# Kernel tuning notes

Hardware: AMD Instinct MI355X
Metric: run time of the kernel (lower is better)

Reference implementation:

```python
import jax, jax.numpy as jnp
import numpy as np

B, T, C = 8, 2048, 1024  # batch, seq_len (== block_size), n_embed
HEAD = 64


def setup_inputs() -> dict:
    key = jax.random.key(0)
    k1, k2, k3, k4 = jax.random.split(key, 4)
    x = jax.random.normal(k1, (B, T, C), dtype=jnp.float32)
    # nn.Linear(n_embed, head_size, bias=False) -> weight [head, C]; stored as [C, head]
    Wk = jax.random.normal(k2, (C, HEAD), dtype=jnp.float32) * (C ** -0.5)
    Wq = jax.random.normal(k3, (C, HEAD), dtype=jnp.float32) * (C ** -0.5)
    Wv = jax.random.normal(k4, (C, HEAD), dtype=jnp.float32) * (C ** -0.5)
    return {"x": x, "Wk": Wk, "Wq": Wq, "Wv": Wv}


def reference(x, Wk, Wq, Wv):
    Bx, Tx, Cx = x.shape
    k = jnp.einsum('btc,ch->bth', x, Wk)  # [B,T,HEAD]
    q = jnp.einsum('btc,ch->bth', x, Wq)
    v = jnp.einsum('btc,ch->bth', x, Wv)
    # Source quirk: scores = k @ q^T (k rows), scaled by n_embed**-0.5 (C, not head_size)
    scores = jnp.einsum('bih,bjh->bij', k, q) * (Cx ** -0.5)  # [B,T,T]
    causal = jnp.tril(jnp.ones((Tx, Tx), dtype=bool))
    scores = jnp.where(causal, scores, -jnp.inf)
    attn = jax.nn.softmax(scores, axis=-1)
    out = jnp.einsum('bij,bjh->bih', attn, v)  # [B,T,HEAD]
    return out
```

## Files before the change

### kernel.cpp

```cpp
#include <hip/hip_runtime.h>
#include <cstdint>

#define B_ 8
#define T_ 2048
#define C_ 1024
#define H_ 64
#define BT_ (B_ * T_)

typedef short short8 __attribute__((ext_vector_type(8)));
typedef short bh4 __attribute__((ext_vector_type(4)));
typedef float f32x4 __attribute__((ext_vector_type(4)));

__device__ inline short f2bf(float f) {
  uint32_t u = __float_as_uint(f);
  u += 0x7fffu + ((u >> 16) & 1u);
  return (short)(u >> 16);
}

__device__ __forceinline__ void gl_lds16(const void* g, void* l) {
  __builtin_amdgcn_global_load_lds(
      (const __attribute__((address_space(1))) unsigned int*)g,
      (__attribute__((address_space(3))) unsigned int*)l, 16, 0, 0);
}

#define ALOADO(dst, p, off)                                        \
  asm volatile("global_load_dwordx4 %0, %1, off offset:" #off      \
               : "=v"(dst) : "v"(p) : "memory")

__global__ __launch_bounds__(256) void prep_w(
    const float* __restrict__ Wk, const float* __restrict__ Wq,
    const float* __restrict__ Wv, short* __restrict__ Wp) {
  __shared__ float wl[64][68];
  const int mat = blockIdx.x >> 4;
  const int kc = blockIdx.x & 15;
  const float* W = (mat == 0) ? Wk : (mat == 1) ? Wq : Wv;
  const float sc = (mat == 0) ? 0.03125f * 1.44269504088896f : 1.0f;
  const int t = threadIdx.x;
  const int k0 = kc * 64;
#pragma unroll
  for (int j = 0; j < 4; ++j) {
    int s = t + 256 * j;
    int kr = s >> 4, cf = s & 15;
    float4 v = *reinterpret_cast<const float4*>(&W[(size_t)(k0 + kr) * H_ + cf * 4]);
    wl[kr][cf * 4 + 0] = v.x; wl[kr][cf * 4 + 1] = v.y;
    wl[kr][cf * 4 + 2] = v.z; wl[kr][cf * 4 + 3] = v.w;
  }
  __syncthreads();
#pragma unroll
  for (int j = 0; j < 2; ++j) {
    int s = t + 256 * j;
    int n = s >> 3, g = s & 7;
    short8 o;
#pragma unroll
    for (int i = 0; i < 8; ++i) o[i] = f2bf(wl[8 * g + i][n] * sc);
    const int ng = mat * 64 + n;
    const int nt = ng >> 4, l15c = ng & 15;
    const int f = g >> 2, lg2 = g & 3;
    short* dst = Wp + (((size_t)(kc * 12 + nt) * 2 + f) << 9) +
                 ((lg2 << 4) + l15c) * 8;
    *reinterpret_cast<short8*>(dst) = o;
  }
}

__global__ __launch_bounds__(256, 1) void proj_kernel(
    const float* __restrict__ x, const short* __restrict__ Wp,
    short* __restrict__ Kp, short* __restrict__ Qp, short* __restrict__ Vt) {
  __shared__ float xs[2][32 * 64];
  const int t = threadIdx.x;
  const int w = t >> 6, lane = t & 63;
  const int l15 = lane & 15, lg = lane >> 4;
  const int rg = w >> 1, ch = w & 1;
  const int rowBase = blockIdx.x * 32;

  f32x4 acc[6];
  const f32x4 zf = {0.f, 0.f, 0.f, 0.f};
#pragma unroll
  for (int i = 0; i < 6; ++i) acc[i] = zf;

  auto stageX = [&](int buf, int k0) {
#pragma unroll
    for (int j = 0; j < 2; ++j) {
      const int seg = w * 2 + j;
      const int r = seg * 4 + (lane >> 4);
      const float* g =
          &x[(size_t)(rowBase + r) * C_ + k0 + (((lane & 15) ^ (r & 7)) << 2)];
      gl_lds16(g, (char*)&xs[buf][0] + seg * 1024);
    }
  };

  stageX(0, 0);

#pragma unroll 1
  for (int it = 0; it < 16; ++it) {
    __syncthreads();
    const int cb = it & 1;
    short8 bw[12];
    const short* wb0 = Wp + (((size_t)(it * 12 + 6 * ch)) << 10) + lane * 8;
    const short* wb1 = wb0 + 2048;
    const short* wb2 = wb0 + 4096;
    ALOADO(bw[0], wb0, 0);    ALOADO(bw[1], wb0, 1024);
    ALOADO(bw[2], wb0, 2048); ALOADO(bw[3], wb0, 3072);
    ALOADO(bw[4], wb1, 0);    ALOADO(bw[5], wb1, 1024);
    ALOADO(bw[6], wb1, 2048); ALOADO(bw[7], wb1, 3072);
    ALOADO(bw[8], wb2, 0);    ALOADO(bw[9], wb2, 1024);
    ALOADO(bw[10], wb2, 2048); ALOADO(bw[11], wb2, 3072);
    __builtin_amdgcn_sched_barrier(0);
    if (it < 15) stageX(cb ^ 1, (it + 1) * 64);
    __builtin_amdgcn_sched_barrier(0);
    if (it < 15) {
      asm volatile("s_waitcnt vmcnt(2)" ::: "memory");
    } else {
      asm volatile("s_waitcnt vmcnt(0)" ::: "memory");
    }
    __builtin_amdgcn_sched_barrier(0);

    const int arow = 16 * rg + l15;
    const int x7 = arow & 7;
    const float* xrow = &xs[cb][arow * 64];
    float4 fa = *reinterpret_cast<const float4*>(xrow + (((2 * lg) ^ x7) << 2));
    float4 fb = *reinterpret_cast<const float4*>(xrow + (((2 * lg + 1) ^ x7) << 2));
    float4 fc = *reinterpret_cast<const float4*>(xrow + (((2 * lg + 8) ^ x7) << 2));
    float4 fd = *reinterpret_cast<const float4*>(xrow + (((2 * lg + 9) ^ x7) << 2));
    short8 a0, a1;
    a0[0] = f2bf(fa.x); a0[1] = f2bf(fa.y); a0[2] = f2bf(fa.z); a0[3] = f2bf(fa.w);
    a0[4] = f2bf(fb.x); a0[5] = f2bf(fb.y); a0[6] = f2bf(fb.z); a0[7] = f2bf(fb.w);
    a1[0] = f2bf(fc.x); a1[1] = f2bf(fc.y); a1[2] = f2bf(fc.z); a1[3] = f2bf(fc.w);
    a1[4] = f2bf(fd.x); a1[5] = f2bf(fd.y); a1[6] = f2bf(fd.z); a1[7] = f2bf(fd.w);
#pragma unroll
    for (int nt = 0; nt < 6; ++nt) {
      acc[nt] = __builtin_amdgcn_mfma_f32_16x16x32_bf16(a0, bw[2 * nt], acc[nt], 0, 0, 0);
      acc[nt] = __builtin_amdgcn_mfma_f32_16x16x32_bf16(a1, bw[2 * nt + 1], acc[nt], 0, 0, 0);
    }
  }

  const int strip = blockIdx.x * 2 + rg;
  const int rb = strip * 16;
#pragma unroll
  for (int nt = 0; nt < 6; ++nt) {
    const int ntg = 6 * ch + nt;
    if (ntg < 8) {
      short* O = (ntg < 4) ? Kp : Qp;
      const int col = (ntg & 3) * 16 + l15;
#pragma unroll
      for (int r = 0; r < 4; ++r)
        O[(size_t)(rb + lg * 4 + r) * H_ + col] = f2bf(acc[nt][r]);
    }
  }
  __syncthreads();
  if (ch == 1) {
    short* vl = reinterpret_cast<short*>(&xs[0][0]) + rg * (16 * 66);
#pragma unroll
    for (int nt = 2; nt < 6; ++nt)
#pragma unroll
      for (int r = 0; r < 4; ++r)
        vl[(lg * 4 + r) * 66 + (nt - 2) * 16 + l15] = f2bf(acc[nt][r]);
    asm volatile("s_waitcnt lgkmcnt(0)" ::: "memory");
    short8 o0, o1;
#pragma unroll
    for (int i = 0; i < 8; ++i) o0[i] = vl[i * 66 + lane];
#pragma unroll
    for (int i = 0; i < 8; ++i) o1[i] = vl[(8 + i) * 66 + lane];
    const int bb = strip >> 7, tb = (strip & 127) * 16;
    short* dst = &Vt[((size_t)bb * H_ + lane) * T_ + tb];
    *reinterpret_cast<short8*>(dst) = o0;
    *reinterpret_cast<short8*>(dst + 8) = o1;
  }
}

__global__ __launch_bounds__(512) void attn_kernel(
    const short* __restrict__ Kq, const short* __restrict__ Qk,
    const short* __restrict__ Vt, float* __restrict__ Pg,
    float* __restrict__ Mg) {
  __shared__ short Ks[4][64 * 64];
  __shared__ short Vs[4][64 * 64];
  const int t = threadIdx.x, w = t >> 6, lane = t & 63;
  const int l15 = lane & 15, lg = lane >> 4;
  const int batch = blockIdx.x & 7;
  const int rest = blockIdx.x >> 3;
  const int qh = rest & 3;
  const int g = rest >> 2;
  const int sidx = (g < 8) ? (15 - g) : (g - 8);
  const int rg = w;
  const short* Kb = Kq + (size_t)batch * T_ * H_;
  const short* Qb = Qk + (size_t)batch * T_ * H_;
  const short* Vb = Vt + (size_t)batch * H_ * T_;
  const f32x4 zf = {0.f, 0.f, 0.f, 0.f};
  const int k7 = l15 & 7;

  const int qbase = sidx * 128;
  const int qrow = qbase + rg * 16 + l15;
  const short8 qa0 = *reinterpret_cast<const short8*>(&Kb[(size_t)qrow * H_ + lg * 8]);
  const short8 qa1 = *reinterpret_cast<const short8*>(&Kb[(size_t)qrow * H_ + lg * 8 + 32]);
  const int ntop = 2 * sidx + 1;
  const int nlist = (ntop >= qh) ? (((ntop - qh) >> 2) + 1) : 0;
  const int np = (nlist + 1) >> 1;

  const int tp = w >> 2, kind = (w >> 1) & 1, q2 = w & 1;
  const int srow = lane >> 3;
  const int ssw = ((lane & 7) ^ srow) << 3;
  auto stage = [&](int per) {
    const int le = 2 * per + tp;
    if (le >= nlist) return;
    const int gkt = 4 * le + qh;
    const int buf = (per & 1) * 2 + tp;
    const int kbase = gkt * 64;
    if (kind == 0) {
#pragma unroll
      for (int g2 = 0; g2 < 4; ++g2) {
        const int gg = q2 * 4 + g2;
        gl_lds16(&Qb[(size_t)(kbase + gg * 8 + srow) * H_ + ssw],
                 (char*)&Ks[buf][0] + gg * 1024);
      }
    } else {
#pragma unroll
      for (int g2 = 0; g2 < 4; ++g2) {
        const int gg = q2 * 4 + g2;
        gl_lds16(&Vb[(size_t)(gg * 8 + srow) * T_ + kbase + ssw],
                 (char*)&Vs[buf][0] + gg * 1024);
      }
    }
  };

  f32x4 O[4];
#pragma unroll
  for (int i = 0; i < 4; ++i) O[i] = zf;
  float m = -1e30f, l = 0.f;

  stage(0);

#pragma unroll 1
  for (int i = 0; i < np; ++i) {
    __syncthreads();
    if (i + 1 < np) stage(i + 1);
#pragma unroll 1
    for (int tt = 0; tt < 2; ++tt) {
      const int le = 2 * i + tt;
      if (le < nlist) {
        const int gkt = 4 * le + qh;
        const int cb = (i & 1) * 2 + tt;
        const int kbase = gkt * 64;
        f32x4 S[4];
        __builtin_amdgcn_s_setprio(1);
#pragma unroll
        for (int nt = 0; nt < 4; ++nt) {
          S[nt] = zf;
          const short* krow = &Ks[cb][(16 * nt + l15) * 64];
          short8 kf0 = *reinterpret_cast<const short8*>(&krow[(lg ^ k7) << 3]);
          short8 kf1 = *reinterpret_cast<const short8*>(&krow[((4 + lg) ^ k7) << 3]);
          S[nt] = __builtin_amdgcn_mfma_f32_16x16x32_bf16(kf0, qa0, S[nt], 0, 0, 0);
          S[nt] = __builtin_amdgcn_mfma_f32_16x16x32_bf16(kf1, qa1, S[nt], 0, 0, 0);
        }
        __builtin_amdgcn_s_setprio(0);
        if (gkt >= 2 * sidx) {
#pragma unroll
          for (int nt = 0; nt < 4; ++nt) {
            const int klo = kbase + 16 * nt + 4 * lg;
#pragma unroll
            for (int r = 0; r < 4; ++r)
              if (klo + r > qrow) S[nt][r] = -1e30f;
          }
        }
        float mx0 = fmaxf(fmaxf(S[0][0], S[0][1]), fmaxf(S[0][2], S[0][3]));
        float mx1 = fmaxf(fmaxf(S[1][0], S[1][1]), fmaxf(S[1][2], S[1][3]));
        float mx2 = fmaxf(fmaxf(S[2][0], S[2][1]), fmaxf(S[2][2], S[2][3]));
        float mx3 = fmaxf(fmaxf(S[3][0], S[3][1]), fmaxf(S[3][2], S[3][3]));
        float mx = fmaxf(fmaxf(mx0, mx1), fmaxf(mx2, mx3));
        mx = fmaxf(mx, __shfl_xor(mx, 16));
        mx = fmaxf(mx, __shfl_xor(mx, 32));
        const float mn = fmaxf(m, mx);
        const float scv = exp2f(m - mn);
        m = mn;
        float rs = 0.f;
#pragma unroll
        for (int nt = 0; nt < 4; ++nt)
#pragma unroll
          for (int r = 0; r < 4; ++r) {
            const float pv = exp2f(S[nt][r] - mn);
            S[nt][r] = pv;
            rs += pv;
          }
        rs += __shfl_xor(rs, 16);
        rs += __shfl_xor(rs, 32);
        l = l * scv + rs;
#pragma unroll
        for (int nt = 0; nt < 4; ++nt) O[nt] *= scv;
        const int d7 = l15 & 7;
        const int vo = 4 * (lg & 1);
        __builtin_amdgcn_s_setprio(1);
#pragma unroll
        for (int kc = 0; kc < 2; ++kc) {
          short8 pa;
#pragma unroll
          for (int jj = 0; jj < 8; ++jj)
            pa[jj] = f2bf(S[2 * kc + (jj >> 2)][jj & 3]);
          const int slo = ((4 * kc + (lg >> 1)) ^ d7) << 3;
          const int shi = ((4 * kc + 2 + (lg >> 1)) ^ d7) << 3;
#pragma unroll
          for (int nt = 0; nt < 4; ++nt) {
            const short* vrow = &Vs[cb][(16 * nt + l15) * 64];
            const bh4 vlo = *reinterpret_cast<const bh4*>(&vrow[slo + vo]);
            const bh4 vhi = *reinterpret_cast<const bh4*>(&vrow[shi + vo]);
            short8 vf;
            vf[0] = vlo[0]; vf[1] = vlo[1]; vf[2] = vlo[2]; vf[3] = vlo[3];
            vf[4] = vhi[0]; vf[5] = vhi[1]; vf[6] = vhi[2]; vf[7] = vhi[3];
            O[nt] = __builtin_amdgcn_mfma_f32_16x16x32_bf16(vf, pa, O[nt], 0, 0, 0);
          }
        }
        __builtin_amdgcn_s_setprio(0);
      }
    }
  }

  const size_t gr = (size_t)batch * T_ + qrow;
#pragma unroll
  for (int nt = 0; nt < 4; ++nt)
    *reinterpret_cast<f32x4*>(&Pg[((size_t)qh * BT_ + gr) * H_ + 16 * nt + 4 * lg]) = O[nt];
  if (lg == 0) {
    Mg[((size_t)qh * BT_ + gr) * 2 + 0] = m;
    Mg[((size_t)qh * BT_ + gr) * 2 + 1] = l;
  }
}

__global__ __launch_bounds__(256) void combine_kernel(
    const float* __restrict__ Pg, const float* __restrict__ Mg,
    float* __restrict__ out) {
  const int t = threadIdx.x;
#pragma unroll
  for (int k = 0; k < 2; ++k) {
    const int task = blockIdx.x * 512 + k * 256 + t;
    const int row = task >> 4;
    const int c4 = task & 15;
    float Mh[4], Lh[4];
#pragma unroll
    for (int h = 0; h < 4; ++h) {
      Mh[h] = Mg[((size_t)h * BT_ + row) * 2 + 0];
      Lh[h] = Mg[((size_t)h * BT_ + row) * 2 + 1];
    }
    const float M = fmaxf(fmaxf(Mh[0], Mh[1]), fmaxf(Mh[2], Mh[3]));
    float L = 0.f;
    f32x4 o = {0.f, 0.f, 0.f, 0.f};
#pragma unroll
    for (int h = 0; h < 4; ++h) {
      const float e = exp2f(Mh[h] - M);
      L += Lh[h] * e;
      const f32x4 po =
          *reinterpret_cast<const f32x4*>(&Pg[((size_t)h * BT_ + row) * H_ + c4 * 4]);
      o += po * e;
    }
    const f32x4 res = o * (1.f / L);
    *reinterpret_cast<f32x4*>(&out[(size_t)row * H_ + c4 * 4]) = res;
  }
}

extern "C" void kernel_launch(void* const* d_in, const int* in_sizes, int n_in,
                              void* d_out, int out_size, void* d_ws, size_t ws_size,
                              hipStream_t stream) {
  const float* x = (const float*)d_in[0];
  const float* Wk = (const float*)d_in[1];
  const float* Wq = (const float*)d_in[2];
  const float* Wv = (const float*)d_in[3];
  float* out = (float*)d_out;

  short* Kp = (short*)d_ws;
  short* Qp = Kp + (size_t)BT_ * H_;
  short* Vt = Qp + (size_t)BT_ * H_;
  short* Wp = Vt + (size_t)BT_ * H_;
  float* Pg = (float*)(Wp + 192 * C_);
  float* Mg = Pg + (size_t)4 * BT_ * H_;

  hipLaunchKernelGGL(prep_w, dim3(48), dim3(256), 0, stream, Wk, Wq, Wv, Wp);
  hipLaunchKernelGGL(proj_kernel, dim3(512), dim3(256), 0, stream, x, Wp, Kp, Qp, Vt);
  hipLaunchKernelGGL(attn_kernel, dim3(512), dim3(512), 0, stream, Kp, Qp, Vt, Pg, Mg);
  hipLaunchKernelGGL(combine_kernel, dim3(512), dim3(256), 0, stream, Pg, Mg, out);
}
```

Measured before the change: 50.33 us.

## Split projection blocks to 16 rows so each wave owns three N tiles

```diff
diff --git a/kernel.cpp b/kernel.cpp
--- a/kernel.cpp
+++ b/kernel.cpp
@@ -65,27 +65,24 @@
 __global__ __launch_bounds__(256, 1) void proj_kernel(
     const float* __restrict__ x, const short* __restrict__ Wp,
     short* __restrict__ Kp, short* __restrict__ Qp, short* __restrict__ Vt) {
-  __shared__ float xs[2][32 * 64];
+  __shared__ float xs[2][16 * 64];
   const int t = threadIdx.x;
   const int w = t >> 6, lane = t & 63;
   const int l15 = lane & 15, lg = lane >> 4;
-  const int rg = w >> 1, ch = w & 1;
-  const int rowBase = blockIdx.x * 32;
-
-  f32x4 acc[6];
+  const int ch = w;
+  const int rowBase = blockIdx.x * 16;
+
+  f32x4 acc[3];
   const f32x4 zf = {0.f, 0.f, 0.f, 0.f};
 #pragma unroll
-  for (int i = 0; i < 6; ++i) acc[i] = zf;
+  for (int i = 0; i < 3; ++i) acc[i] = zf;
 
   auto stageX = [&](int buf, int k0) {
-#pragma unroll
-    for (int j = 0; j < 2; ++j) {
-      const int seg = w * 2 + j;
-      const int r = seg * 4 + (lane >> 4);
-      const float* g =
-          &x[(size_t)(rowBase + r) * C_ + k0 + (((lane & 15) ^ (r & 7)) << 2)];
-      gl_lds16(g, (char*)&xs[buf][0] + seg * 1024);
-    }
+    const int seg = w;
+    const int r = seg * 4 + (lane >> 4);
+    const float* g =
+        &x[(size_t)(rowBase + r) * C_ + k0 + (((lane & 15) ^ (r & 7)) << 2)];
+    gl_lds16(g, (char*)&xs[buf][0] + seg * 1024);
   };
 
   stageX(0, 0);
@@ -94,27 +91,23 @@
   for (int it = 0; it < 16; ++it) {
     __syncthreads();
     const int cb = it & 1;
-    short8 bw[12];
-    const short* wb0 = Wp + (((size_t)(it * 12 + 6 * ch)) << 10) + lane * 8;
-    const short* wb1 = wb0 + 2048;
-    const short* wb2 = wb0 + 4096;
-    ALOADO(bw[0], wb0, 0);    ALOADO(bw[1], wb0, 1024);
-    ALOADO(bw[2], wb0, 2048); ALOADO(bw[3], wb0, 3072);
-    ALOADO(bw[4], wb1, 0);    ALOADO(bw[5], wb1, 1024);
-    ALOADO(bw[6], wb1, 2048); ALOADO(bw[7], wb1, 3072);
-    ALOADO(bw[8], wb2, 0);    ALOADO(bw[9], wb2, 1024);
-    ALOADO(bw[10], wb2, 2048); ALOADO(bw[11], wb2, 3072);
+    short8 bw[6];
+    const short* wb = Wp + (((size_t)(it * 12 + 3 * ch)) << 10) + lane * 8;
+    const short* wb2 = wb + 2048;
+    ALOADO(bw[0], wb, 0);    ALOADO(bw[1], wb, 1024);
+    ALOADO(bw[2], wb, 2048); ALOADO(bw[3], wb, 3072);
+    ALOADO(bw[4], wb2, 0);   ALOADO(bw[5], wb2, 1024);
     __builtin_amdgcn_sched_barrier(0);
     if (it < 15) stageX(cb ^ 1, (it + 1) * 64);
     __builtin_amdgcn_sched_barrier(0);
     if (it < 15) {
-      asm volatile("s_waitcnt vmcnt(2)" ::: "memory");
+      asm volatile("s_waitcnt vmcnt(1)" ::: "memory");
     } else {
       asm volatile("s_waitcnt vmcnt(0)" ::: "memory");
     }
     __builtin_amdgcn_sched_barrier(0);
 
-    const int arow = 16 * rg + l15;
+    const int arow = l15;
     const int x7 = arow & 7;
     const float* xrow = &xs[cb][arow * 64];
     float4 fa = *reinterpret_cast<const float4*>(xrow + (((2 * lg) ^ x7) << 2));
@@ -127,34 +120,32 @@
     a1[0] = f2bf(fc.x); a1[1] = f2bf(fc.y); a1[2] = f2bf(fc.z); a1[3] = f2bf(fc.w);
     a1[4] = f2bf(fd.x); a1[5] = f2bf(fd.y); a1[6] = f2bf(fd.z); a1[7] = f2bf(fd.w);
 #pragma unroll
-    for (int nt = 0; nt < 6; ++nt) {
+    for (int nt = 0; nt < 3; ++nt) {
       acc[nt] = __builtin_amdgcn_mfma_f32_16x16x32_bf16(a0, bw[2 * nt], acc[nt], 0, 0, 0);
       acc[nt] = __builtin_amdgcn_mfma_f32_16x16x32_bf16(a1, bw[2 * nt + 1], acc[nt], 0, 0, 0);
     }
   }
 
-  const int strip = blockIdx.x * 2 + rg;
+  const int strip = blockIdx.x;
   const int rb = strip * 16;
-#pragma unroll
-  for (int nt = 0; nt < 6; ++nt) {
-    const int ntg = 6 * ch + nt;
+  __shared__ short vl[16 * 66];
+#pragma unroll
+  for (int nt = 0; nt < 3; ++nt) {
+    const int ntg = 3 * ch + nt;
     if (ntg < 8) {
       short* O = (ntg < 4) ? Kp : Qp;
       const int col = (ntg & 3) * 16 + l15;
 #pragma unroll
       for (int r = 0; r < 4; ++r)
         O[(size_t)(rb + lg * 4 + r) * H_ + col] = f2bf(acc[nt][r]);
+    } else {
+#pragma unroll
+      for (int r = 0; r < 4; ++r)
+        vl[(lg * 4 + r) * 66 + (ntg - 8) * 16 + l15] = f2bf(acc[nt][r]);
     }
   }
   __syncthreads();
-  if (ch == 1) {
-    short* vl = reinterpret_cast<short*>(&xs[0][0]) + rg * (16 * 66);
-#pragma unroll
-    for (int nt = 2; nt < 6; ++nt)
-#pragma unroll
-      for (int r = 0; r < 4; ++r)
-        vl[(lg * 4 + r) * 66 + (nt - 2) * 16 + l15] = f2bf(acc[nt][r]);
-    asm volatile("s_waitcnt lgkmcnt(0)" ::: "memory");
+  if (w == 0) {
     short8 o0, o1;
 #pragma unroll
     for (int i = 0; i < 8; ++i) o0[i] = vl[i * 66 + lane];
@@ -369,7 +360,7 @@
   float* Mg = Pg + (size_t)4 * BT_ * H_;
 
   hipLaunchKernelGGL(prep_w, dim3(48), dim3(256), 0, stream, Wk, Wq, Wv, Wp);
-  hipLaunchKernelGGL(proj_kernel, dim3(512), dim3(256), 0, stream, x, Wp, Kp, Qp, Vt);
+  hipLaunchKernelGGL(proj_kernel, dim3(1024), dim3(256), 0, stream, x, Wp, Kp, Qp, Vt);
   hipLaunchKernelGGL(attn_kernel, dim3(512), dim3(512), 0, stream, Kp, Qp, Vt, Pg, Mg);
   hipLaunchKernelGGL(combine_kernel, dim3(512), dim3(256), 0, stream, Pg, Mg, out);
 }
```

Result: slower. 55.22 us (+9.7%).

## Triple-buffer x staging in projection kernel with two-deep prefetch

Applied to the files above, without the earlier changes.

```diff
diff --git a/kernel.cpp b/kernel.cpp
--- a/kernel.cpp
+++ b/kernel.cpp
@@ -65,7 +65,7 @@
 __global__ __launch_bounds__(256, 1) void proj_kernel(
     const float* __restrict__ x, const short* __restrict__ Wp,
     short* __restrict__ Kp, short* __restrict__ Qp, short* __restrict__ Vt) {
-  __shared__ float xs[2][32 * 64];
+  __shared__ float xs[3][32 * 64];
   const int t = threadIdx.x;
   const int w = t >> 6, lane = t & 63;
   const int l15 = lane & 15, lg = lane >> 4;
@@ -77,46 +77,49 @@
 #pragma unroll
   for (int i = 0; i < 6; ++i) acc[i] = zf;
 
-  auto stageX = [&](int buf, int k0) {
+  auto xissue = [&](int s) {
+    const int buf = s % 3;
 #pragma unroll
     for (int j = 0; j < 2; ++j) {
       const int seg = w * 2 + j;
       const int r = seg * 4 + (lane >> 4);
       const float* g =
-          &x[(size_t)(rowBase + r) * C_ + k0 + (((lane & 15) ^ (r & 7)) << 2)];
+          &x[(size_t)(rowBase + r) * C_ + s * 64 + (((lane & 15) ^ (r & 7)) << 2)];
       gl_lds16(g, (char*)&xs[buf][0] + seg * 1024);
     }
   };
-
-  stageX(0, 0);
+  auto wissue = [&](short8* d, int c) {
+    const short* wb0 = Wp + (((size_t)(c * 12 + 6 * ch)) << 10) + lane * 8;
+    const short* wb1 = wb0 + 2048;
+    const short* wb2 = wb0 + 4096;
+    ALOADO(d[0], wb0, 0);    ALOADO(d[1], wb0, 1024);
+    ALOADO(d[2], wb0, 2048); ALOADO(d[3], wb0, 3072);
+    ALOADO(d[4], wb1, 0);    ALOADO(d[5], wb1, 1024);
+    ALOADO(d[6], wb1, 2048); ALOADO(d[7], wb1, 3072);
+    ALOADO(d[8], wb2, 0);    ALOADO(d[9], wb2, 1024);
+    ALOADO(d[10], wb2, 2048); ALOADO(d[11], wb2, 3072);
+  };
+
+  xissue(0);
+  xissue(1);
+  asm volatile("s_waitcnt vmcnt(2)" ::: "memory");
+  __builtin_amdgcn_sched_barrier(0);
+  __builtin_amdgcn_s_barrier();
+  __builtin_amdgcn_sched_barrier(0);
 
 #pragma unroll 1
   for (int it = 0; it < 16; ++it) {
-    __syncthreads();
-    const int cb = it & 1;
     short8 bw[12];
-    const short* wb0 = Wp + (((size_t)(it * 12 + 6 * ch)) << 10) + lane * 8;
-    const short* wb1 = wb0 + 2048;
-    const short* wb2 = wb0 + 4096;
-    ALOADO(bw[0], wb0, 0);    ALOADO(bw[1], wb0, 1024);
-    ALOADO(bw[2], wb0, 2048); ALOADO(bw[3], wb0, 3072);
-    ALOADO(bw[4], wb1, 0);    ALOADO(bw[5], wb1, 1024);
-    ALOADO(bw[6], wb1, 2048); ALOADO(bw[7], wb1, 3072);
-    ALOADO(bw[8], wb2, 0);    ALOADO(bw[9], wb2, 1024);
-    ALOADO(bw[10], wb2, 2048); ALOADO(bw[11], wb2, 3072);
+    wissue(bw, it);
+    const int sn = (it + 2 < 16) ? it + 2 : 15;
+    xissue(sn);
     __builtin_amdgcn_sched_barrier(0);
-    if (it < 15) stageX(cb ^ 1, (it + 1) * 64);
-    __builtin_amdgcn_sched_barrier(0);
-    if (it < 15) {
-      asm volatile("s_waitcnt vmcnt(2)" ::: "memory");
-    } else {
-      asm volatile("s_waitcnt vmcnt(0)" ::: "memory");
-    }
+    asm volatile("s_waitcnt vmcnt(2)" ::: "memory");
     __builtin_amdgcn_sched_barrier(0);
 
     const int arow = 16 * rg + l15;
     const int x7 = arow & 7;
-    const float* xrow = &xs[cb][arow * 64];
+    const float* xrow = &xs[it % 3][arow * 64];
     float4 fa = *reinterpret_cast<const float4*>(xrow + (((2 * lg) ^ x7) << 2));
     float4 fb = *reinterpret_cast<const float4*>(xrow + (((2 * lg + 1) ^ x7) << 2));
     float4 fc = *reinterpret_cast<const float4*>(xrow + (((2 * lg + 8) ^ x7) << 2));
@@ -126,12 +129,19 @@
     a0[4] = f2bf(fb.x); a0[5] = f2bf(fb.y); a0[6] = f2bf(fb.z); a0[7] = f2bf(fb.w);
     a1[0] = f2bf(fc.x); a1[1] = f2bf(fc.y); a1[2] = f2bf(fc.z); a1[3] = f2bf(fc.w);
     a1[4] = f2bf(fd.x); a1[5] = f2bf(fd.y); a1[6] = f2bf(fd.z); a1[7] = f2bf(fd.w);
+    __builtin_amdgcn_s_setprio(1);
 #pragma unroll
     for (int nt = 0; nt < 6; ++nt) {
       acc[nt] = __builtin_amdgcn_mfma_f32_16x16x32_bf16(a0, bw[2 * nt], acc[nt], 0, 0, 0);
       acc[nt] = __builtin_amdgcn_mfma_f32_16x16x32_bf16(a1, bw[2 * nt + 1], acc[nt], 0, 0, 0);
     }
-  }
+    __builtin_amdgcn_s_setprio(0);
+    __builtin_amdgcn_sched_barrier(0);
+    __builtin_amdgcn_s_barrier();
+    __builtin_amdgcn_sched_barrier(0);
+  }
+  asm volatile("s_waitcnt vmcnt(0)" ::: "memory");
+  __builtin_amdgcn_sched_barrier(0);
 
   const int strip = blockIdx.x * 2 + rg;
   const int rb = strip * 16;
```

New measurement: 50.82 us. Within noise of the previous version (+1.0%).
